# Kernel tuning notes

Hardware: AMD Instinct MI355X
Metric: run time of the kernel (lower is better)

## Reference

```python
import jax, jax.numpy as jnp
import numpy as np

N = 2_097_152          # n_transitions = n_envs * buffer_size
GAMMA = 0.99
GAE_LAMBDA = 0.95
CLIP_EPS = 0.2
NORM_ADVANTAGES = True


def setup_inputs() -> dict:
    key = jax.random.key(0)
    ks = jax.random.split(key, 7)
    f = lambda k: jax.random.normal(k, (N, 1), dtype=jnp.float32)
    return {
        "rewards": f(ks[0]),
        "values": f(ks[1]),
        "next_values": f(ks[2]),
        "log_probs": -jnp.abs(f(ks[3])),       # log-probs are <= 0
        "old_log_probs": -jnp.abs(f(ks[4])),
        "terminated": jax.random.randint(ks[5], (N, 1), 0, 2).astype(bool),
        "truncated": jax.random.randint(ks[6], (N, 1), 0, 2).astype(bool),
    }


def reference(rewards, values, next_values, log_probs, old_log_probs,
              terminated, truncated):
    dtype = rewards.dtype
    dones = jnp.logical_or(terminated, truncated)
    not_term = 1.0 - terminated.astype(dtype)          # [N,1]
    not_done = 1.0 - dones.astype(dtype)               # [N,1]

    # TD residuals: delta_n = r_n + gamma * (1 - terminated_n) * V(s'_n) - V(s_n)
    deltas = rewards + GAMMA * not_term * next_values - values   # [N,1]

    # Reverse GAE recurrence (the torch Python for-loop, fused into one scan):
    # adv_n = (1 - done_n) * gamma * lambda * adv_{n+1} + delta_n
    coef = not_done[:, 0] * (GAMMA * GAE_LAMBDA)       # [N]

    def step(adv, cd):
        c, d = cd
        adv = c * adv + d
        return adv, adv

    _, advantages = jax.lax.scan(step, jnp.zeros((), dtype),
                                 (coef, deltas[:, 0]), reverse=True)
    advantages = advantages[:, None]                   # [N,1]

    lambda_returns = advantages + values               # [N,1]

    if NORM_ADVANTAGES:
        # torch .std() is the unbiased (ddof=1) estimator
        adv_n = (advantages - advantages.mean()) / (
            jnp.std(advantages, ddof=1) + 1e-9)
    else:
        adv_n = advantages

    # PPO clipped surrogate, per-sample (the .mean() is a trivial reduction)
    ratio = jnp.exp(log_probs - old_log_probs)
    clamped = jnp.clip(ratio, 1.0 - CLIP_EPS, 1.0 + CLIP_EPS)
    per_sample_actor_loss = -jnp.minimum(ratio * adv_n, clamped * adv_n)

    # [N,3]: normalized advantages, lambda returns, per-sample clipped objective
    return jnp.concatenate([adv_n, lambda_returns, per_sample_actor_loss], axis=1)
```

## Files before the change

### kernel.cpp

```cpp
#include <hip/hip_runtime.h>
#include <stdint.h>

static constexpr int BLOCK = 256;
static constexpr int ITEMS = 8;
static constexpr int CHUNK = BLOCK * ITEMS;
static constexpr int MAXNB = 1024;

#define GAMMA_F 0.99f
static __device__ __forceinline__ float gl_const() { return (float)(0.99 * 0.95); }

__device__ __forceinline__ void compose(float& a1, float& b1, float a2, float b2) {
    b1 = fmaf(a1, b2, b1);
    a1 = a1 * a2;
}

__device__ __forceinline__ int detect_mode(const void* term, int n_elems, int* flg) {
    int t = threadIdx.x;
    if (t == 0) { flg[0] = 0; flg[1] = 0; }
    __syncthreads();
    if (t < 256) {
        const unsigned char* p = (const unsigned char*)term;
        int i0 = 4 * t;
        if (i0 + 3 < n_elems) {
            unsigned b1 = p[i0 + 1], b2 = p[i0 + 2], b3 = p[i0 + 3];
            if (b1) atomicOr(&flg[0], 1);
            if (b2 | b3) atomicOr(&flg[1], 1);
        }
    }
    __syncthreads();
    return flg[0] ? 1 : (flg[1] ? 2 : 0);
}

__device__ __forceinline__ int load_bool1(const void* p, long i, int mode) {
    if (mode == 1) return ((const unsigned char*)p)[i] != 0;
    if (mode == 0) return ((const int*)p)[i] != 0;
    return ((const float*)p)[i] != 0.0f;
}

__device__ __forceinline__ void load_bool8(const void* p, long base, int mode, int* f) {
    if (mode == 1) {
        uint2 q = *(const uint2*)((const unsigned char*)p + base);
        unsigned w[2] = {q.x, q.y};
#pragma unroll
        for (int j = 0; j < 8; ++j) f[j] = (int)((w[j >> 2] >> ((j & 3) * 8)) & 0xffu);
    } else if (mode == 0) {
        const int4* q = (const int4*)((const int*)p + base);
#pragma unroll
        for (int k = 0; k < 2; ++k) {
            int4 v = q[k];
            f[4*k] = v.x; f[4*k+1] = v.y; f[4*k+2] = v.z; f[4*k+3] = v.w;
        }
    } else {
        const float4* q = (const float4*)((const float*)p + base);
#pragma unroll
        for (int k = 0; k < 2; ++k) {
            float4 v = q[k];
            f[4*k] = v.x != 0.f; f[4*k+1] = v.y != 0.f; f[4*k+2] = v.z != 0.f; f[4*k+3] = v.w != 0.f;
        }
    }
}

__device__ __forceinline__ void compute_cd(
    const float* __restrict__ rewards, const float* __restrict__ values,
    const float* __restrict__ next_values, const void* __restrict__ term,
    const void* __restrict__ trunc, int mode, long base, int n,
    float* c, float* d, float* v)
{
    const float GL = gl_const();
    if (base + ITEMS <= n) {
        float r[ITEMS], nv[ITEMS];
        const float4* r4 = (const float4*)(rewards + base);
        const float4* v4 = (const float4*)(values + base);
        const float4* n4 = (const float4*)(next_values + base);
#pragma unroll
        for (int k = 0; k < 2; ++k) {
            float4 a = r4[k]; r[4*k]=a.x; r[4*k+1]=a.y; r[4*k+2]=a.z; r[4*k+3]=a.w;
            float4 b = v4[k]; v[4*k]=b.x; v[4*k+1]=b.y; v[4*k+2]=b.z; v[4*k+3]=b.w;
            float4 q = n4[k]; nv[4*k]=q.x; nv[4*k+1]=q.y; nv[4*k+2]=q.z; nv[4*k+3]=q.w;
        }
        int tm[ITEMS], tr[ITEMS];
        load_bool8(term,  base, mode, tm);
        load_bool8(trunc, base, mode, tr);
#pragma unroll
        for (int j = 0; j < ITEMS; ++j) {
            float nt = tm[j] ? 0.f : 1.f;
            float nd = (tm[j] | tr[j]) ? 0.f : 1.f;
            d[j] = r[j] + GAMMA_F * nt * nv[j] - v[j];
            c[j] = nd * GL;
        }
    } else {
#pragma unroll
        for (int j = 0; j < ITEMS; ++j) {
            long i = base + j;
            if (i < (long)n) {
                int tm = load_bool1(term, i, mode);
                int tr = load_bool1(trunc, i, mode);
                float nt = tm ? 0.f : 1.f;
                float nd = (tm | tr) ? 0.f : 1.f;
                v[j] = values[i];
                d[j] = rewards[i] + GAMMA_F * nt * next_values[i] - v[j];
                c[j] = nd * GL;
            } else { c[j] = 1.f; d[j] = 0.f; v[j] = 0.f; }
        }
    }
}

__global__ __launch_bounds__(BLOCK) void k1_agg(
    const float* __restrict__ rewards, const float* __restrict__ values,
    const float* __restrict__ next_values, const void* __restrict__ term,
    const void* __restrict__ trunc, float2* __restrict__ blockAgg,
    float2* __restrict__ E2, float4* __restrict__ bs4, float* __restrict__ bs1,
    int n)
{
    __shared__ int flg[2];
    __shared__ float wA[4], wB[4];
    __shared__ float red[4][5];

    const int t = threadIdx.x;
    const int lane = t & 63, w = t >> 6;
    const int bid = blockIdx.x;
    const int mode = detect_mode(term, n, flg);
    const long base = (long)bid * CHUNK + (long)t * ITEMS;

    float c[ITEMS], d[ITEMS], v[ITEMS];
    compute_cd(rewards, values, next_values, term, trunc, mode, base, n, c, d, v);

    float a = 1.f, b = 0.f;
#pragma unroll
    for (int j = ITEMS - 1; j >= 0; --j) { b = fmaf(c[j], b, d[j]); a *= c[j]; }

#pragma unroll
    for (int dd = 1; dd < 64; dd <<= 1) {
        float ra = __shfl_down(a, dd, 64);
        float rb = __shfl_down(b, dd, 64);
        if (lane + dd < 64) { b = fmaf(a, rb, b); a *= ra; }
    }
    if (lane == 0) { wA[w] = a; wB[w] = b; }
    float ea = __shfl_down(a, 1, 64);
    float eb = __shfl_down(b, 1, 64);
    if (lane == 63) { ea = 1.f; eb = 0.f; }
    __syncthreads();
    for (int ww = w + 1; ww < 4; ++ww) compose(ea, eb, wA[ww], wB[ww]);
    if (t == 0) {
        float Aa = wA[0], Ab = wB[0];
        for (int ww = 1; ww < 4; ++ww) compose(Aa, Ab, wA[ww], wB[ww]);
        blockAgg[bid] = make_float2(Aa, Ab);
    }
    E2[(long)bid * BLOCK + t] = make_float2(ea, eb);

    float p = ea, q = eb;
    float sP = 0.f, sQ = 0.f, sP2 = 0.f, sPQ = 0.f, sQ2 = 0.f;
#pragma unroll
    for (int j = ITEMS - 1; j >= 0; --j) {
        p = c[j] * p;
        q = fmaf(c[j], q, d[j]);
        if (base + j < (long)n) {
            sP += p; sQ += q; sP2 += p*p; sPQ += p*q; sQ2 += q*q;
        }
    }
#pragma unroll
    for (int dd = 32; dd > 0; dd >>= 1) {
        sP  += __shfl_down(sP,  dd, 64);
        sQ  += __shfl_down(sQ,  dd, 64);
        sP2 += __shfl_down(sP2, dd, 64);
        sPQ += __shfl_down(sPQ, dd, 64);
        sQ2 += __shfl_down(sQ2, dd, 64);
    }
    if (lane == 0) { red[w][0]=sP; red[w][1]=sQ; red[w][2]=sP2; red[w][3]=sPQ; red[w][4]=sQ2; }
    __syncthreads();
    if (t == 0) {
        float m0=0,m1=0,m2=0,m3=0,m4=0;
        for (int ww = 0; ww < 4; ++ww) { m0+=red[ww][0]; m1+=red[ww][1]; m2+=red[ww][2]; m3+=red[ww][3]; m4+=red[ww][4]; }
        bs4[bid] = make_float4(m0, m1, m2, m3);
        bs1[bid] = m4;
    }
}

__global__ __launch_bounds__(BLOCK) void k2_scan(
    const float2* __restrict__ blockAgg, const float4* __restrict__ bs4,
    const float* __restrict__ bs1, float* __restrict__ S,
    float* __restrict__ stats, int nb, int n)
{
    __shared__ float sA[BLOCK], sB[BLOCK];
    __shared__ double dS[BLOCK], dS2[BLOCK];
    const int t = threadIdx.x;
    float la[4], lb[4];
#pragma unroll
    for (int j = 0; j < 4; ++j) {
        int i = 4 * t + j;
        if (i < nb) { float2 f = blockAgg[i]; la[j] = f.x; lb[j] = f.y; }
        else        { la[j] = 1.f; lb[j] = 0.f; }
    }
    float a = 1.f, b = 0.f;
#pragma unroll
    for (int j = 3; j >= 0; --j) { b = fmaf(la[j], b, lb[j]); a *= la[j]; }
    sA[t] = a; sB[t] = b;
    __syncthreads();
    for (int dd = 1; dd < BLOCK; dd <<= 1) {
        float ra = 1.f, rb = 0.f;
        if (t + dd < BLOCK) { ra = sA[t + dd]; rb = sB[t + dd]; }
        __syncthreads();
        b = fmaf(a, rb, b);
        a *= ra;
        sA[t] = a; sB[t] = b;
        __syncthreads();
    }
    float x = (t + 1 < BLOCK) ? sB[t + 1] : 0.f;
    double ds = 0.0, ds2 = 0.0;
#pragma unroll
    for (int j = 3; j >= 0; --j) {
        int i = 4 * t + j;
        if (i < nb) {
            S[i] = x;
            float4 s4 = bs4[i];
            double xd = (double)x;
            ds  += (double)s4.x * xd + (double)s4.y;
            ds2 += (double)s4.z * xd * xd + 2.0 * (double)s4.w * xd + (double)bs1[i];
        }
        x = fmaf(la[j], x, lb[j]);
    }
    dS[t] = ds; dS2[t] = ds2;
    __syncthreads();
    for (int dd = BLOCK / 2; dd > 0; dd >>= 1) {
        if (t < dd) { dS[t] += dS[t + dd]; dS2[t] += dS2[t + dd]; }
        __syncthreads();
    }
    if (t == 0) {
        double sum = dS[0], sumsq = dS2[0];
        double mean = sum / (double)n;
        double var = (sumsq - sum * sum / (double)n) / (double)(n - 1);
        if (var < 0.0) var = 0.0;
        stats[0] = (float)mean;
        stats[1] = 1.0f / ((float)sqrt(var) + 1e-9f);
    }
}

__global__ __launch_bounds__(BLOCK) void k3_final(
    const float* __restrict__ rewards, const float* __restrict__ values,
    const float* __restrict__ next_values, const void* __restrict__ term,
    const void* __restrict__ trunc, const float* __restrict__ lp,
    const float* __restrict__ olp, const float2* __restrict__ E2,
    const float* __restrict__ S, const float* __restrict__ stats,
    float* __restrict__ out, int n)
{
    __shared__ int flg[2];
    const int t = threadIdx.x;
    const int bid = blockIdx.x;
    const int mode = detect_mode(term, n, flg);
    const long base = (long)bid * CHUNK + (long)t * ITEMS;

    float c[ITEMS], d[ITEMS], v[ITEMS];
    compute_cd(rewards, values, next_values, term, trunc, mode, base, n, c, d, v);

    float2 e = E2[(long)bid * BLOCK + t];
    float x = fmaf(e.x, S[bid], e.y);
    float adv[ITEMS];
#pragma unroll
    for (int j = ITEMS - 1; j >= 0; --j) {
        x = fmaf(c[j], x, d[j]);
        adv[j] = x;
    }
    const float mean = stats[0];
    const float inv  = stats[1];
    if (base + ITEMS <= n) {
        float l[ITEMS], o[ITEMS];
        const float4* l4 = (const float4*)(lp + base);
        const float4* o4 = (const float4*)(olp + base);
#pragma unroll
        for (int k = 0; k < 2; ++k) {
            float4 q = l4[k]; l[4*k]=q.x; l[4*k+1]=q.y; l[4*k+2]=q.z; l[4*k+3]=q.w;
            float4 w = o4[k]; o[4*k]=w.x; o[4*k+1]=w.y; o[4*k+2]=w.z; o[4*k+3]=w.w;
        }
        float buf[3 * ITEMS];
#pragma unroll
        for (int j = 0; j < ITEMS; ++j) {
            float an = (adv[j] - mean) * inv;
            float ratio = expf(l[j] - o[j]);
            float cl = fminf(fmaxf(ratio, 0.8f), 1.2f);
            buf[3*j]     = an;
            buf[3*j + 1] = adv[j] + v[j];
            buf[3*j + 2] = -fminf(ratio * an, cl * an);
        }
        float4* dst = (float4*)(out + 3 * base);
#pragma unroll
        for (int k = 0; k < 6; ++k)
            dst[k] = make_float4(buf[4*k], buf[4*k+1], buf[4*k+2], buf[4*k+3]);
    } else {
        for (int j = 0; j < ITEMS; ++j) {
            long i = base + j;
            if (i < (long)n) {
                float an = (adv[j] - mean) * inv;
                float ratio = expf(lp[i] - olp[i]);
                float cl = fminf(fmaxf(ratio, 0.8f), 1.2f);
                out[3*i]     = an;
                out[3*i + 1] = adv[j] + v[j];
                out[3*i + 2] = -fminf(ratio * an, cl * an);
            }
        }
    }
}

extern "C" void kernel_launch(void* const* d_in, const int* in_sizes, int n_in,
                              void* d_out, int out_size, void* d_ws, size_t ws_size,
                              hipStream_t stream) {
    const float* rewards     = (const float*)d_in[0];
    const float* values      = (const float*)d_in[1];
    const float* next_values = (const float*)d_in[2];
    const float* lp          = (const float*)d_in[3];
    const float* olp         = (const float*)d_in[4];
    const void*  term        = d_in[5];
    const void*  trunc       = d_in[6];
    float* out = (float*)d_out;
    int n = in_sizes[0];
    int nb = (n + CHUNK - 1) / CHUNK;

    char* ws = (char*)d_ws;
    float2* blockAgg = (float2*)ws;
    float4* bs4      = (float4*)(ws + MAXNB * 8);
    float*  bs1      = (float*) (ws + MAXNB * 8 + MAXNB * 16);
    float*  S        = (float*) (ws + MAXNB * 8 + MAXNB * 16 + MAXNB * 4);
    float*  stats    = (float*) (ws + MAXNB * 8 + MAXNB * 16 + MAXNB * 8);
    float2* E2       = (float2*)(ws + MAXNB * 8 + MAXNB * 16 + MAXNB * 8 + 256);

    k1_agg <<<nb, BLOCK, 0, stream>>>(rewards, values, next_values, term, trunc,
                                      blockAgg, E2, bs4, bs1, n);
    k2_scan<<<1,  BLOCK, 0, stream>>>(blockAgg, bs4, bs1, S, stats, nb, n);
    k3_final<<<nb, BLOCK, 0, stream>>>(rewards, values, next_values, term, trunc,
                                       lp, olp, E2, S, stats, out, n);
}
```

Baseline: 130.5 us.

## Fuse single-block cross-block scan into final kernel, recomputed redundantly per block

```diff
diff --git a/kernel.cpp b/kernel.cpp
--- a/kernel.cpp
+++ b/kernel.cpp
@@ -176,14 +176,29 @@
     }
 }
 
-__global__ __launch_bounds__(BLOCK) void k2_scan(
+__global__ __launch_bounds__(BLOCK) void k3_final(
+    const float* __restrict__ rewards, const float* __restrict__ values,
+    const float* __restrict__ next_values, const void* __restrict__ term,
+    const void* __restrict__ trunc, const float* __restrict__ lp,
+    const float* __restrict__ olp, const float2* __restrict__ E2,
     const float2* __restrict__ blockAgg, const float4* __restrict__ bs4,
-    const float* __restrict__ bs1, float* __restrict__ S,
-    float* __restrict__ stats, int nb, int n)
+    const float* __restrict__ bs1, float* __restrict__ out, int n, int nb)
 {
+    __shared__ int flg[2];
     __shared__ float sA[BLOCK], sB[BLOCK];
+    __shared__ float sS[MAXNB];
     __shared__ double dS[BLOCK], dS2[BLOCK];
+    __shared__ float statMean, statInv;
+
     const int t = threadIdx.x;
+    const int bid = blockIdx.x;
+    const int mode = detect_mode(term, n, flg);
+    const long base = (long)bid * CHUNK + (long)t * ITEMS;
+
+    float c[ITEMS], d[ITEMS], v[ITEMS];
+    compute_cd(rewards, values, next_values, term, trunc, mode, base, n, c, d, v);
+    float2 e = E2[(long)bid * BLOCK + t];
+
     float la[4], lb[4];
 #pragma unroll
     for (int j = 0; j < 4; ++j) {
@@ -211,7 +226,7 @@
     for (int j = 3; j >= 0; --j) {
         int i = 4 * t + j;
         if (i < nb) {
-            S[i] = x;
+            sS[i] = x;
             float4 s4 = bs4[i];
             double xd = (double)x;
             ds  += (double)s4.x * xd + (double)s4.y;
@@ -230,38 +245,20 @@
         double mean = sum / (double)n;
         double var = (sumsq - sum * sum / (double)n) / (double)(n - 1);
         if (var < 0.0) var = 0.0;
-        stats[0] = (float)mean;
-        stats[1] = 1.0f / ((float)sqrt(var) + 1e-9f);
-    }
-}
-
-__global__ __launch_bounds__(BLOCK) void k3_final(
-    const float* __restrict__ rewards, const float* __restrict__ values,
-    const float* __restrict__ next_values, const void* __restrict__ term,
-    const void* __restrict__ trunc, const float* __restrict__ lp,
-    const float* __restrict__ olp, const float2* __restrict__ E2,
-    const float* __restrict__ S, const float* __restrict__ stats,
-    float* __restrict__ out, int n)
-{
-    __shared__ int flg[2];
-    const int t = threadIdx.x;
-    const int bid = blockIdx.x;
-    const int mode = detect_mode(term, n, flg);
-    const long base = (long)bid * CHUNK + (long)t * ITEMS;
-
-    float c[ITEMS], d[ITEMS], v[ITEMS];
-    compute_cd(rewards, values, next_values, term, trunc, mode, base, n, c, d, v);
-
-    float2 e = E2[(long)bid * BLOCK + t];
-    float x = fmaf(e.x, S[bid], e.y);
+        statMean = (float)mean;
+        statInv  = 1.0f / ((float)sqrt(var) + 1e-9f);
+    }
+    __syncthreads();
+
+    float xx = fmaf(e.x, sS[bid], e.y);
     float adv[ITEMS];
 #pragma unroll
     for (int j = ITEMS - 1; j >= 0; --j) {
-        x = fmaf(c[j], x, d[j]);
-        adv[j] = x;
-    }
-    const float mean = stats[0];
-    const float inv  = stats[1];
+        xx = fmaf(c[j], xx, d[j]);
+        adv[j] = xx;
+    }
+    const float mean = statMean;
+    const float inv  = statInv;
     if (base + ITEMS <= n) {
         float l[ITEMS], o[ITEMS];
         const float4* l4 = (const float4*)(lp + base);
@@ -318,13 +315,10 @@
     float2* blockAgg = (float2*)ws;
     float4* bs4      = (float4*)(ws + MAXNB * 8);
     float*  bs1      = (float*) (ws + MAXNB * 8 + MAXNB * 16);
-    float*  S        = (float*) (ws + MAXNB * 8 + MAXNB * 16 + MAXNB * 4);
-    float*  stats    = (float*) (ws + MAXNB * 8 + MAXNB * 16 + MAXNB * 8);
-    float2* E2       = (float2*)(ws + MAXNB * 8 + MAXNB * 16 + MAXNB * 8 + 256);
+    float2* E2       = (float2*)(ws + MAXNB * 8 + MAXNB * 16 + MAXNB * 4 + 256);
 
     k1_agg <<<nb, BLOCK, 0, stream>>>(rewards, values, next_values, term, trunc,
                                       blockAgg, E2, bs4, bs1, n);
-    k2_scan<<<1,  BLOCK, 0, stream>>>(blockAgg, bs4, bs1, S, stats, nb, n);
     k3_final<<<nb, BLOCK, 0, stream>>>(rewards, values, next_values, term, trunc,
-                                       lp, olp, E2, S, stats, out, n);
-}
+                                       lp, olp, E2, blockAgg, bs4, bs1, out, n, nb);
+}
```

After: 130.1 us. About the same (-0.3%).
